# Kernel tuning notes

Hardware: AMD Instinct MI355X
Metric: run time of the kernel (lower is better)

Reference implementation:

```python
import jax, jax.numpy as jnp
import numpy as np
from jax import lax

BATCH, SEQ, D_FSQ = 8, 4096, 4
D_MODEL, D_STATE, D_CONV, L, OUT = 256, 16, 4, 2, 2
D_INNER = 2 * D_MODEL  # expand=2
EPS = 1e-5


def setup_inputs() -> dict:
    key = jax.random.key(0)
    ks = jax.random.split(key, 10)
    s = 0.02
    return {
        "z_seq": jax.random.normal(ks[0], (BATCH, SEQ, D_FSQ), jnp.float32),
        "ip_w": jax.random.normal(ks[1], (D_MODEL, D_FSQ), jnp.float32) * s,
        "ip_b": jnp.zeros((D_MODEL,), jnp.float32),
        "norm_g": jnp.ones((L, D_MODEL), jnp.float32),
        "norm_b": jnp.zeros((L, D_MODEL), jnp.float32),
        "inproj_w": jax.random.normal(ks[2], (L, 2 * D_INNER, D_MODEL), jnp.float32) * s,
        "conv_w": jax.random.normal(ks[3], (L, D_INNER, D_CONV), jnp.float32) * s,
        "conv_b": jnp.zeros((L, D_INNER), jnp.float32),
        "xproj_w": jax.random.normal(ks[4], (L, 2 * D_STATE + 1, D_INNER), jnp.float32) * s,
        "dt_w": jax.random.normal(ks[5], (L, D_INNER), jnp.float32) * s,
        "dt_b": jnp.zeros((L, D_INNER), jnp.float32),
        "outproj_w": jax.random.normal(ks[6], (L, D_MODEL, D_INNER), jnp.float32) * s,
        "onorm_g": jnp.ones((D_MODEL,), jnp.float32),
        "onorm_b": jnp.zeros((D_MODEL,), jnp.float32),
        "op_w": jax.random.normal(ks[7], (OUT, D_MODEL), jnp.float32) * s,
        "op_b": jnp.zeros((OUT,), jnp.float32),
    }


def _layernorm(x, g, b):
    mu = jnp.mean(x, axis=-1, keepdims=True)
    var = jnp.mean(jnp.square(x - mu), axis=-1, keepdims=True)
    return (x - mu) * lax.rsqrt(var + EPS) * g + b


def _selective_scan(x, dt, Bm, Cm):
    # x, dt: [B,T,d_inner]; Bm, Cm: [B,T,d_state]
    A = -jnp.arange(1, D_STATE + 1, dtype=x.dtype)  # [d_state]

    def step(h, inp):
        x_t, dt_t, B_t, C_t = inp  # [B,di],[B,di],[B,ds],[B,ds]
        A_bar = jnp.exp(dt_t[:, :, None] * A)            # [B,di,ds]
        h = A_bar * h + (dt_t * x_t)[:, :, None] * B_t[:, None, :]
        y_t = jnp.einsum("bds,bs->bd", h, C_t)
        return h, y_t

    xs = (jnp.swapaxes(x, 0, 1), jnp.swapaxes(dt, 0, 1),
          jnp.swapaxes(Bm, 0, 1), jnp.swapaxes(Cm, 0, 1))
    h0 = jnp.zeros((x.shape[0], D_INNER, D_STATE), x.dtype)
    _, ys = lax.scan(step, h0, xs)
    return jnp.swapaxes(ys, 0, 1)  # [B,T,d_inner]


def _block(x, g, b, Wi, cw, cb, Wx, dw, db, Wo):
    res = x
    x = _layernorm(x, g, b)
    xz = x @ Wi.T                               # [B,T,2*d_inner]
    xp, z = xz[..., :D_INNER], xz[..., D_INNER:]
    # causal depthwise conv1d (padding=d_conv-1 then truncate == left pad)
    xc = lax.conv_general_dilated(
        jnp.swapaxes(xp, 1, 2), cw[:, None, :], window_strides=(1,),
        padding=[(D_CONV - 1, 0)], dimension_numbers=("NCH", "OIH", "NCH"),
        feature_group_count=D_INNER) + cb[None, :, None]
    xc = jax.nn.silu(jnp.swapaxes(xc, 1, 2))    # [B,T,d_inner]
    ssm = xc @ Wx.T                             # [B,T,2*ds+1]
    Bm = ssm[..., :D_STATE]
    Cm = ssm[..., D_STATE:2 * D_STATE]
    dt_raw = ssm[..., 2 * D_STATE:]             # [B,T,1]
    dt = jax.nn.softplus(dt_raw * dw + db)      # Linear(1, d_inner)
    y = _selective_scan(xc, dt, Bm, Cm)
    y = y * jax.nn.silu(z)
    y = y @ Wo.T
    return y + res


def reference(z_seq, ip_w, ip_b, norm_g, norm_b, inproj_w, conv_w, conv_b,
              xproj_w, dt_w, dt_b, outproj_w, onorm_g, onorm_b, op_w, op_b):
    x = z_seq @ ip_w.T + ip_b
    for l in range(L):
        x = _block(x, norm_g[l], norm_b[l], inproj_w[l], conv_w[l], conv_b[l],
                   xproj_w[l], dt_w[l], dt_b[l], outproj_w[l])
    x = _layernorm(x, onorm_g, onorm_b)
    return x @ op_w.T + op_b
```

## Files before the change

kernel.cpp:

```cpp
#include <hip/hip_runtime.h>
#include <cstddef>
#include <cstdint>

#define DEV __device__ __forceinline__

namespace {
constexpr int BATCH = 8;
constexpr int SEQL  = 4096;
constexpr int DM    = 256;
constexpr int DS    = 16;
constexpr int DI    = 512;
constexpr int NTOK  = BATCH * SEQL;
constexpr int TC    = 64;
constexpr int NCH   = SEQL / TC;
constexpr float EPSF = 1e-5f;

constexpr size_t OFF_X   = 0;
constexpr size_t OFF_XPB = OFF_X   + (size_t)NTOK * DM * 4;
constexpr size_t OFF_ZBB = OFF_XPB + (size_t)NTOK * DI * 2;
constexpr size_t OFF_XCB = OFF_ZBB + (size_t)NTOK * DI * 2;
constexpr size_t OFF_XLN = OFF_XCB + (size_t)NTOK * DI * 2;
constexpr size_t OFF_B   = OFF_XLN + (size_t)NTOK * DM * 2;
constexpr size_t OFF_C   = OFF_B   + (size_t)NTOK * DS * 4;
constexpr size_t OFF_DTR = OFF_C   + (size_t)NTOK * DS * 4;
constexpr size_t OFF_HE  = OFF_DTR + (size_t)NTOK * 4;
constexpr size_t OFF_DTC = OFF_HE  + (size_t)BATCH * DI * NCH * DS * 4;
constexpr size_t OFF_WBI = OFF_DTC + (size_t)BATCH * DI * NCH * 4;
constexpr size_t OFF_WBO = OFF_WBI + (size_t)2 * 2 * DI * DM * 2;
constexpr size_t OFF_WBX = OFF_WBO + (size_t)2 * DM * DI * 2;
constexpr size_t OFF_CWT = OFF_WBX + (size_t)2 * 48 * DI * 2;
constexpr size_t WBI_EL  = 2 * 2 * DI * DM;
constexpr size_t WBO_EL  = 2 * DM * DI;
}

typedef __attribute__((ext_vector_type(8))) short short8;
typedef __attribute__((ext_vector_type(4))) float f32x4;

DEV float sigmoidf_(float v) { return 1.0f / (1.0f + __expf(-v)); }
DEV float siluf_(float v)    { return v * sigmoidf_(v); }
DEV float softplusf_(float v) {
    return fmaxf(v, 0.0f) + __logf(1.0f + __expf(-fabsf(v)));
}
DEV float b2f(unsigned short u) {
    union { unsigned int i; float f; } c; c.i = ((unsigned int)u) << 16; return c.f;
}
DEV float4 b4f(ushort4 u) {
    return make_float4(b2f(u.x), b2f(u.y), b2f(u.z), b2f(u.w));
}
DEV unsigned short f2b(float f) {
    union { float f; unsigned int i; } c; c.f = f;
    unsigned int lsb = (c.i >> 16) & 1u;
    c.i += 0x7fffu + lsb;
    return (unsigned short)(c.i >> 16);
}
DEV void pows16(float p, float* pb) {
    float p2 = p * p, p4 = p2 * p2, p8 = p4 * p4;
    pb[0] = p;        pb[1] = p2;       pb[2] = p2 * p;      pb[3] = p4;
    pb[4] = p4 * p;   pb[5] = p4 * p2;  pb[6] = p4 * p2 * p; pb[7] = p8;
    pb[8] = p8 * p;   pb[9] = p8 * p2;  pb[10] = p8 * p2 * p; pb[11] = p8 * p4;
    pb[12] = p8 * p4 * p; pb[13] = p8 * p4 * p2; pb[14] = p8 * p4 * p2 * p; pb[15] = p8 * p8;
}
DEV void gload_lds16(const unsigned short* g, unsigned short* l) {
    __builtin_amdgcn_global_load_lds(
        (__attribute__((address_space(1))) void*)(g),
        (__attribute__((address_space(3))) void*)(l), 16, 0, 0);
}

__global__ void k_cvt(const float* __restrict__ src, unsigned short* __restrict__ dst, int n) {
    int g = (blockIdx.x * 256 + threadIdx.x) * 4;
    if (g >= n) return;
    float4 v = *(const float4*)(src + g);
    ushort4 o;
    o.x = f2b(v.x); o.y = f2b(v.y); o.z = f2b(v.z); o.w = f2b(v.w);
    *(ushort4*)(dst + g) = o;
}

__global__ void k_cvtx(const float* __restrict__ src, unsigned short* __restrict__ dst) {
    int idx = blockIdx.x * 256 + threadIdx.x;
    int l = idx / (48 * 512), r = (idx >> 9) % 48, cc = idx & 511;
    dst[idx] = (r < 33) ? f2b(src[(size_t)(l * 33 + r) * 512 + cc]) : (unsigned short)0;
}

__global__ void k_cvtc(const float* __restrict__ src, float* __restrict__ dst) {
    int idx = blockIdx.x * 256 + threadIdx.x;
    int l = idx >> 11, k = (idx >> 9) & 3, d = idx & 511;
    dst[idx] = src[(size_t)(l * DI + d) * 4 + k];
}

__global__ void k_inproj(const float* __restrict__ z, const float* __restrict__ w,
                         const float* __restrict__ bias, float* __restrict__ x) {
    int g = blockIdx.x * 256 + threadIdx.x;
    int i = g >> 8, m = g & 255;
    float4 zv = *(const float4*)(z + (size_t)i * 4);
    float4 wv = *(const float4*)(w + (size_t)m * 4);
    float r = bias[m];
    r = fmaf(zv.x, wv.x, r);
    r = fmaf(zv.y, wv.y, r);
    r = fmaf(zv.z, wv.z, r);
    r = fmaf(zv.w, wv.w, r);
    x[g] = r;
}

__global__ void k_lnrow(const float* __restrict__ x, const float* __restrict__ gam,
                        const float* __restrict__ bet, unsigned short* __restrict__ xln) {
    int lane = threadIdx.x & 63, wid = threadIdx.x >> 6;
    int i = blockIdx.x * 4 + wid;
    float4 v = *(const float4*)(x + (size_t)i * DM + lane * 4);
    float s = v.x + v.y + v.z + v.w;
    float q = v.x * v.x + v.y * v.y + v.z * v.z + v.w * v.w;
    #pragma unroll
    for (int m = 32; m; m >>= 1) { s += __shfl_xor(s, m, 64); q += __shfl_xor(q, m, 64); }
    float mu = s * (1.0f / DM);
    float rs = rsqrtf(q * (1.0f / DM) - mu * mu + EPSF);
    float4 g4 = *(const float4*)(gam + lane * 4);
    float4 b4 = *(const float4*)(bet + lane * 4);
    ushort4 o;
    o.x = f2b((v.x - mu) * rs * g4.x + b4.x);
    o.y = f2b((v.y - mu) * rs * g4.y + b4.y);
    o.z = f2b((v.z - mu) * rs * g4.z + b4.z);
    o.w = f2b((v.w - mu) * rs * g4.w + b4.w);
    *(ushort4*)(xln + (size_t)i * DM + lane * 4) = o;
}

__global__ __launch_bounds__(256) void k_gemm1(
    const unsigned short* __restrict__ A, const unsigned short* __restrict__ W,
    unsigned short* __restrict__ xpb, unsigned short* __restrict__ zbb) {
    __shared__ unsigned short As[128 * 32];
    __shared__ unsigned short Bs[128 * 32];
    int tid = threadIdx.x, lane = tid & 63, wid = tid >> 6;
    int tileN = blockIdx.x & 7, tileM = blockIdx.x >> 3;
    int i0 = tileM * 128, n0 = tileN * 128;
    f32x4 acc[4][4];
    #pragma unroll
    for (int mi = 0; mi < 4; mi++)
        #pragma unroll
        for (int ni = 0; ni < 4; ni++) acc[mi][ni] = (f32x4){0.f, 0.f, 0.f, 0.f};

    int srow = (wid << 5) + (lane >> 2);
    int sblk = lane & 3;
    const unsigned short* ga = A + (size_t)(i0 + srow) * 256 + sblk * 8;
    const unsigned short* gb = W + (size_t)(n0 + srow) * 256 + sblk * 8;
    unsigned short* la = As + (wid << 5) * 32;
    unsigned short* lb = Bs + (wid << 5) * 32;
    int ar = lane & 15, ab = lane >> 4;
    const short8* pa = (const short8*)(As + ((wid >> 1) * 64 + ar) * 32 + ab * 8);
    const short8* pb = (const short8*)(Bs + ((wid & 1) * 64 + ar) * 32 + ab * 8);

    for (int k0 = 0; k0 < 256; k0 += 32) {
        gload_lds16(ga + k0,            la);
        gload_lds16(ga + k0 + 16 * 256, la + 16 * 32);
        gload_lds16(gb + k0,            lb);
        gload_lds16(gb + k0 + 16 * 256, lb + 16 * 32);
        __syncthreads();
        short8 a[4], b[4];
        #pragma unroll
        for (int mi = 0; mi < 4; mi++) a[mi] = pa[mi * 64];
        #pragma unroll
        for (int ni = 0; ni < 4; ni++) b[ni] = pb[ni * 64];
        #pragma unroll
        for (int mi = 0; mi < 4; mi++)
            #pragma unroll
            for (int ni = 0; ni < 4; ni++)
                acc[mi][ni] = __builtin_amdgcn_mfma_f32_16x16x32_bf16(a[mi], b[ni], acc[mi][ni], 0, 0, 0);
        __syncthreads();
    }
    int wr = wid >> 1, wc = wid & 1;
    int rbase = i0 + wr * 64 + (lane >> 4) * 4;
    int cbase = n0 + wc * 64 + (lane & 15);
    unsigned short* dst = (n0 < 512) ? xpb : zbb;
    int coff = (n0 < 512) ? cbase : cbase - 512;
    #pragma unroll
    for (int mi = 0; mi < 4; mi++)
        #pragma unroll
        for (int ni = 0; ni < 4; ni++)
            #pragma unroll
            for (int j = 0; j < 4; j++)
                dst[(size_t)(rbase + mi * 16 + j) * 512 + coff + ni * 16] = f2b(acc[mi][ni][j]);
}

__global__ void k_conv(const unsigned short* __restrict__ xpb, const float* __restrict__ cwT,
                       const float* __restrict__ cb, unsigned short* __restrict__ xcb) {
    int g = blockIdx.x * 256 + threadIdx.x;
    int tg = g >> 7, dq = g & 127;
    int d = dq * 4;
    int i0 = tg * 8;
    float4 w0 = *(const float4*)(cwT + 0 * DI + d);
    float4 w1 = *(const float4*)(cwT + 1 * DI + d);
    float4 w2 = *(const float4*)(cwT + 2 * DI + d);
    float4 w3 = *(const float4*)(cwT + 3 * DI + d);
    float4 bi = *(const float4*)(cb + d);
    float4 x0, x1, x2;
    if ((i0 & (SEQL - 1)) != 0) {
        x0 = b4f(*(const ushort4*)(xpb + (size_t)(i0 - 3) * DI + d));
        x1 = b4f(*(const ushort4*)(xpb + (size_t)(i0 - 2) * DI + d));
        x2 = b4f(*(const ushort4*)(xpb + (size_t)(i0 - 1) * DI + d));
    } else {
        x0 = x1 = x2 = make_float4(0.f, 0.f, 0.f, 0.f);
    }
    #pragma unroll
    for (int tt = 0; tt < 8; tt++) {
        float4 xc = b4f(*(const ushort4*)(xpb + (size_t)(i0 + tt) * DI + d));
        float4 a = bi;
        a.x = fmaf(w0.x, x0.x, a.x); a.y = fmaf(w0.y, x0.y, a.y);
        a.z = fmaf(w0.z, x0.z, a.z); a.w = fmaf(w0.w, x0.w, a.w);
        a.x = fmaf(w1.x, x1.x, a.x); a.y = fmaf(w1.y, x1.y, a.y);
        a.z = fmaf(w1.z, x1.z, a.z); a.w = fmaf(w1.w, x1.w, a.w);
        a.x = fmaf(w2.x, x2.x, a.x); a.y = fmaf(w2.y, x2.y, a.y);
        a.z = fmaf(w2.z, x2.z, a.z); a.w = fmaf(w2.w, x2.w, a.w);
        a.x = fmaf(w3.x, xc.x, a.x); a.y = fmaf(w3.y, xc.y, a.y);
        a.z = fmaf(w3.z, xc.z, a.z); a.w = fmaf(w3.w, xc.w, a.w);
        ushort4 o;
        o.x = f2b(siluf_(a.x)); o.y = f2b(siluf_(a.y));
        o.z = f2b(siluf_(a.z)); o.w = f2b(siluf_(a.w));
        *(ushort4*)(xcb + (size_t)(i0 + tt) * DI + d) = o;
        x0 = x1; x1 = x2; x2 = xc;
    }
}

__global__ __launch_bounds__(256) void k_xprojm(
    const unsigned short* __restrict__ A, const unsigned short* __restrict__ W,
    float* __restrict__ Bm, float* __restrict__ Cm, float* __restrict__ dtr) {
    __shared__ unsigned short As[128 * 32];
    __shared__ unsigned short Bs[48 * 32];
    int tid = threadIdx.x, lane = tid & 63, wid = tid >> 6;
    int i0 = blockIdx.x * 128;
    f32x4 acc[2][3];
    #pragma unroll
    for (int mi = 0; mi < 2; mi++)
        #pragma unroll
        for (int ni = 0; ni < 3; ni++) acc[mi][ni] = (f32x4){0.f, 0.f, 0.f, 0.f};

    int srow = lane >> 2, sblk = lane & 3;
    const unsigned short* ga = A + (size_t)(i0 + (wid << 5) + srow) * 512 + sblk * 8;
    unsigned short* la = As + (wid << 5) * 32;
    const unsigned short* gb = W + (size_t)((wid << 4) + srow) * 512 + sblk * 8;
    unsigned short* lb = Bs + (wid << 4) * 32;
    int ar = lane & 15, ab = lane >> 4;

    for (int k0 = 0; k0 < 512; k0 += 32) {
        gload_lds16(ga + k0,            la);
        gload_lds16(ga + k0 + 16 * 512, la + 16 * 32);
        if (wid < 3) gload_lds16(gb + k0, lb);
        __syncthreads();
        short8 a[2], b[3];
        #pragma unroll
        for (int mi = 0; mi < 2; mi++)
            a[mi] = *(const short8*)(As + ((wid << 5) + mi * 16 + ar) * 32 + ab * 8);
        #pragma unroll
        for (int ni = 0; ni < 3; ni++)
            b[ni] = *(const short8*)(Bs + (ni * 16 + ar) * 32 + ab * 8);
        #pragma unroll
        for (int mi = 0; mi < 2; mi++)
            #pragma unroll
            for (int ni = 0; ni < 3; ni++)
                acc[mi][ni] = __builtin_amdgcn_mfma_f32_16x16x32_bf16(a[mi], b[ni], acc[mi][ni], 0, 0, 0);
        __syncthreads();
    }
    #pragma unroll
    for (int mi = 0; mi < 2; mi++)
        #pragma unroll
        for (int ni = 0; ni < 3; ni++)
            #pragma unroll
            for (int j = 0; j < 4; j++) {
                int row = i0 + (wid << 5) + mi * 16 + (lane >> 4) * 4 + j;
                int ng = ni * 16 + (lane & 15);
                float v = acc[mi][ni][j];
                if (ng < 16)       Bm[(size_t)row * DS + ng] = v;
                else if (ng < 32)  Cm[(size_t)row * DS + ng - 16] = v;
                else if (ng == 32) dtr[row] = v;
            }
}

__global__ __launch_bounds__(256) void k_scan1(
    const unsigned short* __restrict__ xcb, const float* __restrict__ Bm,
    const float* __restrict__ dtr, const float* __restrict__ dw,
    const float* __restrict__ db, float* __restrict__ hend, float* __restrict__ dtc) {
    __shared__ float Bsh[64][16];
    __shared__ float dtl[64];
    int tid = threadIdx.x;
    int blk = blockIdx.x;
    int half = blk & 1, c = (blk >> 1) & (NCH - 1), b = blk >> 7;
    int d = half * 256 + tid;
    int i0 = (b << 12) + c * TC;
    if (tid < 64) dtl[tid] = dtr[i0 + tid];
    {
        int idx = tid * 4, tt = idx >> 4, ss = idx & 15;
        *(float4*)(&Bsh[tt][ss]) = *(const float4*)(Bm + (size_t)(i0 + tt) * DS + ss);
    }
    __syncthreads();
    float dwd = dw[d], dbd = db[d];
    float h[16];
    #pragma unroll
    for (int s = 0; s < 16; s++) h[s] = 0.0f;
    float dtsum = 0.0f;
    for (int t = 0; t < TC; t++) {
        float dt = softplusf_(fmaf(dtl[t], dwd, dbd));
        dtsum += dt;
        float p = __expf(-dt);
        float pb[16];
        pows16(p, pb);
        float x = b2f(xcb[(size_t)(i0 + t) * DI + d]);
        float dtx = dt * x;
        float Bv[16];
        *(float4*)(Bv + 0)  = *(const float4*)(&Bsh[t][0]);
        *(float4*)(Bv + 4)  = *(const float4*)(&Bsh[t][4]);
        *(float4*)(Bv + 8)  = *(const float4*)(&Bsh[t][8]);
        *(float4*)(Bv + 12) = *(const float4*)(&Bsh[t][12]);
        #pragma unroll
        for (int s = 0; s < 16; s++) h[s] = fmaf(pb[s], h[s], dtx * Bv[s]);
    }
    size_t hb = ((size_t)(b * DI + d) * NCH + c) * DS;
    #pragma unroll
    for (int s = 0; s < 16; s += 4)
        *(float4*)(hend + hb + s) = make_float4(h[s], h[s + 1], h[s + 2], h[s + 3]);
    dtc[(size_t)(b * DI + d) * NCH + c] = dtsum;
}

__global__ void k_scan2(float* __restrict__ hend, const float* __restrict__ dtc) {
    int g = blockIdx.x * 256 + threadIdx.x;
    int s = g & 15, dd = (g >> 4) & 511, b = g >> 13;
    size_t base = (size_t)(b * DI + dd) * NCH;
    float hin = 0.0f;
    float kneg = -(float)(s + 1);
    #pragma unroll 4
    for (int c = 0; c < NCH; c++) {
        size_t a = (base + c) * DS + s;
        float tmp = hend[a];
        float pb = __expf(kneg * dtc[base + c]);
        hend[a] = hin;
        hin = fmaf(pb, hin, tmp);
    }
}

__global__ __launch_bounds__(256) void k_scan3(
    const unsigned short* __restrict__ xcb, const float* __restrict__ Bm,
    const float* __restrict__ Cm, const float* __restrict__ dtr,
    const float* __restrict__ dw, const float* __restrict__ db,
    const float* __restrict__ hend, const unsigned short* __restrict__ zbb,
    unsigned short* __restrict__ ygb) {
    __shared__ float Bsh[64][16];
    __shared__ float Csh[64][16];
    __shared__ float dtl[64];
    int tid = threadIdx.x;
    int blk = blockIdx.x;
    int half = blk & 1, c = (blk >> 1) & (NCH - 1), b = blk >> 7;
    int d = half * 256 + tid;
    int i0 = (b << 12) + c * TC;
    if (tid < 64) dtl[tid] = dtr[i0 + tid];
    {
        int idx = tid * 4, tt = idx >> 4, ss = idx & 15;
        *(float4*)(&Bsh[tt][ss]) = *(const float4*)(Bm + (size_t)(i0 + tt) * DS + ss);
        *(float4*)(&Csh[tt][ss]) = *(const float4*)(Cm + (size_t)(i0 + tt) * DS + ss);
    }
    __syncthreads();
    float dwd = dw[d], dbd = db[d];
    float h[16];
    size_t hb = ((size_t)(b * DI + d) * NCH + c) * DS;
    #pragma unroll
    for (int s = 0; s < 16; s += 4) *(float4*)(h + s) = *(const float4*)(hend + hb + s);
    for (int t = 0; t < TC; t++) {
        float dt = softplusf_(fmaf(dtl[t], dwd, dbd));
        float p = __expf(-dt);
        float pb[16];
        pows16(p, pb);
        size_t gi = (size_t)(i0 + t) * DI + d;
        float x = b2f(xcb[gi]);
        float dtx = dt * x;
        float Bv[16], Cv[16];
        *(float4*)(Bv + 0)  = *(const float4*)(&Bsh[t][0]);
        *(float4*)(Bv + 4)  = *(const float4*)(&Bsh[t][4]);
        *(float4*)(Bv + 8)  = *(const float4*)(&Bsh[t][8]);
        *(float4*)(Bv + 12) = *(const float4*)(&Bsh[t][12]);
        *(float4*)(Cv + 0)  = *(const float4*)(&Csh[t][0]);
        *(float4*)(Cv + 4)  = *(const float4*)(&Csh[t][4]);
        *(float4*)(Cv + 8)  = *(const float4*)(&Csh[t][8]);
        *(float4*)(Cv + 12) = *(const float4*)(&Csh[t][12]);
        float y = 0.0f;
        #pragma unroll
        for (int s = 0; s < 16; s++) {
            h[s] = fmaf(pb[s], h[s], dtx * Bv[s]);
            y = fmaf(h[s], Cv[s], y);
        }
        float z = b2f(zbb[gi]);
        ygb[gi] = f2b(y * siluf_(z));
    }
}

__global__ __launch_bounds__(256) void k_outproj(
    const unsigned short* __restrict__ A, const unsigned short* __restrict__ W,
    float* __restrict__ x) {
    __shared__ unsigned short As[128 * 32];
    __shared__ unsigned short Bs[128 * 32];
    int tid = threadIdx.x, lane = tid & 63, wid = tid >> 6;
    int tileN = blockIdx.x & 1, tileM = blockIdx.x >> 1;
    int i0 = tileM * 128, n0 = tileN * 128;
    f32x4 acc[4][4];
    #pragma unroll
    for (int mi = 0; mi < 4; mi++)
        #pragma unroll
        for (int ni = 0; ni < 4; ni++) acc[mi][ni] = (f32x4){0.f, 0.f, 0.f, 0.f};

    int srow = (wid << 5) + (lane >> 2);
    int sblk = lane & 3;
    const unsigned short* ga = A + (size_t)(i0 + srow) * 512 + sblk * 8;
    const unsigned short* gb = W + (size_t)(n0 + srow) * 512 + sblk * 8;
    unsigned short* la = As + (wid << 5) * 32;
    unsigned short* lb = Bs + (wid << 5) * 32;
    int ar = lane & 15, ab = lane >> 4;
    const short8* pa = (const short8*)(As + ((wid >> 1) * 64 + ar) * 32 + ab * 8);
    const short8* pb = (const short8*)(Bs + ((wid & 1) * 64 + ar) * 32 + ab * 8);

    for (int k0 = 0; k0 < 512; k0 += 32) {
        gload_lds16(ga + k0,            la);
        gload_lds16(ga + k0 + 16 * 512, la + 16 * 32);
        gload_lds16(gb + k0,            lb);
        gload_lds16(gb + k0 + 16 * 512, lb + 16 * 32);
        __syncthreads();
        short8 a[4], b[4];
        #pragma unroll
        for (int mi = 0; mi < 4; mi++) a[mi] = pa[mi * 64];
        #pragma unroll
        for (int ni = 0; ni < 4; ni++) b[ni] = pb[ni * 64];
        #pragma unroll
        for (int mi = 0; mi < 4; mi++)
            #pragma unroll
            for (int ni = 0; ni < 4; ni++)
                acc[mi][ni] = __builtin_amdgcn_mfma_f32_16x16x32_bf16(a[mi], b[ni], acc[mi][ni], 0, 0, 0);
        __syncthreads();
    }
    int wr = wid >> 1, wc = wid & 1;
    int rbase = i0 + wr * 64 + (lane >> 4) * 4;
    int cbase = n0 + wc * 64 + (lane & 15);
    #pragma unroll
    for (int mi = 0; mi < 4; mi++)
        #pragma unroll
        for (int ni = 0; ni < 4; ni++)
            #pragma unroll
            for (int j = 0; j < 4; j++) {
                size_t idx = (size_t)(rbase + mi * 16 + j) * DM + cbase + ni * 16;
                x[idx] += acc[mi][ni][j];
            }
}

__global__ void k_final(const float* __restrict__ x, const float* __restrict__ gam,
                        const float* __restrict__ bet, const float* __restrict__ w,
                        const float* __restrict__ bias, float* __restrict__ out) {
    int lane = threadIdx.x & 63, wid = threadIdx.x >> 6;
    int i = blockIdx.x * 4 + wid;
    float4 v = *(const float4*)(x + (size_t)i * DM + lane * 4);
    float s = v.x + v.y + v.z + v.w;
    float q = v.x * v.x + v.y * v.y + v.z * v.z + v.w * v.w;
    #pragma unroll
    for (int m = 32; m; m >>= 1) { s += __shfl_xor(s, m, 64); q += __shfl_xor(q, m, 64); }
    float mu = s * (1.0f / DM);
    float rs = rsqrtf(q * (1.0f / DM) - mu * mu + EPSF);
    float4 gg = *(const float4*)(gam + lane * 4);
    float4 bb = *(const float4*)(bet + lane * 4);
    float xn[4] = {(v.x - mu) * rs * gg.x + bb.x, (v.y - mu) * rs * gg.y + bb.y,
                   (v.z - mu) * rs * gg.z + bb.z, (v.w - mu) * rs * gg.w + bb.w};
    float4 w0 = *(const float4*)(w + lane * 4);
    float4 w1 = *(const float4*)(w + DM + lane * 4);
    float p0 = xn[0] * w0.x + xn[1] * w0.y + xn[2] * w0.z + xn[3] * w0.w;
    float p1 = xn[0] * w1.x + xn[1] * w1.y + xn[2] * w1.z + xn[3] * w1.w;
    #pragma unroll
    for (int m = 32; m; m >>= 1) { p0 += __shfl_xor(p0, m, 64); p1 += __shfl_xor(p1, m, 64); }
    if (lane == 0) {
        out[(size_t)i * 2]     = p0 + bias[0];
        out[(size_t)i * 2 + 1] = p1 + bias[1];
    }
}

extern "C" void kernel_launch(void* const* d_in, const int* in_sizes, int n_in,
                              void* d_out, int out_size, void* d_ws, size_t ws_size,
                              hipStream_t stream) {
    const float* z_seq     = (const float*)d_in[0];
    const float* ip_w      = (const float*)d_in[1];
    const float* ip_b      = (const float*)d_in[2];
    const float* norm_g    = (const float*)d_in[3];
    const float* norm_b    = (const float*)d_in[4];
    const float* inproj_w  = (const float*)d_in[5];
    const float* conv_w    = (const float*)d_in[6];
    const float* conv_b    = (const float*)d_in[7];
    const float* xproj_w   = (const float*)d_in[8];
    const float* dt_w      = (const float*)d_in[9];
    const float* dt_b      = (const float*)d_in[10];
    const float* outproj_w = (const float*)d_in[11];
    const float* onorm_g   = (const float*)d_in[12];
    const float* onorm_b   = (const float*)d_in[13];
    const float* op_w      = (const float*)d_in[14];
    const float* op_b      = (const float*)d_in[15];

    char* ws = (char*)d_ws;
    float* x    = (float*)(ws + OFF_X);
    unsigned short* xpb = (unsigned short*)(ws + OFF_XPB);
    unsigned short* zbb = (unsigned short*)(ws + OFF_ZBB);
    unsigned short* xcb = (unsigned short*)(ws + OFF_XCB);
    unsigned short* xln = (unsigned short*)(ws + OFF_XLN);
    float* Bmb  = (float*)(ws + OFF_B);
    float* Cmb  = (float*)(ws + OFF_C);
    float* dtrb = (float*)(ws + OFF_DTR);
    float* hend = (float*)(ws + OFF_HE);
    float* dtc  = (float*)(ws + OFF_DTC);
    unsigned short* WbI = (unsigned short*)(ws + OFF_WBI);
    unsigned short* WbO = (unsigned short*)(ws + OFF_WBO);
    unsigned short* WbX = (unsigned short*)(ws + OFF_WBX);
    float* cwT  = (float*)(ws + OFF_CWT);

    k_cvt<<<(int)(WBI_EL / 4 / 256), 256, 0, stream>>>(inproj_w,  WbI, (int)WBI_EL);
    k_cvt<<<(int)(WBO_EL / 4 / 256), 256, 0, stream>>>(outproj_w, WbO, (int)WBO_EL);
    k_cvtx<<<2 * 48 * 512 / 256, 256, 0, stream>>>(xproj_w, WbX);
    k_cvtc<<<2 * 4 * 512 / 256, 256, 0, stream>>>(conv_w, cwT);

    k_inproj<<<NTOK * DM / 256, 256, 0, stream>>>(z_seq, ip_w, ip_b, x);

    for (int l = 0; l < 2; l++) {
        k_lnrow<<<NTOK / 4, 256, 0, stream>>>(x, norm_g + l * DM, norm_b + l * DM, xln);
        k_gemm1<<<(NTOK / 128) * 8, 256, 0, stream>>>(
            xln, WbI + (size_t)l * 2 * DI * DM, xpb, zbb);
        k_conv<<<(NTOK / 8) * 128 / 256, 256, 0, stream>>>(
            xpb, cwT + (size_t)l * 4 * DI, conv_b + (size_t)l * DI, xcb);
        k_xprojm<<<NTOK / 128, 256, 0, stream>>>(
            xcb, WbX + (size_t)l * 48 * DI, Bmb, Cmb, dtrb);
        k_scan1<<<BATCH * NCH * 2, 256, 0, stream>>>(
            xcb, Bmb, dtrb, dt_w + l * DI, dt_b + l * DI, hend, dtc);
        k_scan2<<<BATCH * DI * DS / 256, 256, 0, stream>>>(hend, dtc);
        k_scan3<<<BATCH * NCH * 2, 256, 0, stream>>>(
            xcb, Bmb, Cmb, dtrb, dt_w + l * DI, dt_b + l * DI, hend, zbb, xpb);
        k_outproj<<<(NTOK / 128) * 2, 256, 0, stream>>>(
            xpb, WbO + (size_t)l * DM * DI, x);
    }
    k_final<<<NTOK / 4, 256, 0, stream>>>(x, onorm_g, onorm_b, op_w, op_b, (float*)d_out);
}
```

Before: 509.0 us.

## Halve scan chunk length, process two channels per thread, fuse softplus with decay

The scan chunk length drops from 64 to 32, which doubles the number of chunks. Each scan thread now handles two adjacent channels, using vectorized ushort2 loads and stores for x, z and y, and one launch covers all 512 channels per chunk. Softplus and the exp(-dt) decay are now computed together as p = rcp(1+e^a) and dt = -log(p), which saves a transcendental per step. In exchange, register pressure goes up, and the serial inter-chunk pass in k_scan2 runs twice as long. The fused formula can also lose precision or overflow for large dt arguments.

```diff
diff --git a/kernel.cpp b/kernel.cpp
--- a/kernel.cpp
+++ b/kernel.cpp
@@ -11,7 +11,7 @@
 constexpr int DS    = 16;
 constexpr int DI    = 512;
 constexpr int NTOK  = BATCH * SEQL;
-constexpr int TC    = 64;
+constexpr int TC    = 32;
 constexpr int NCH   = SEQL / TC;
 constexpr float EPSF = 1e-5f;
 
@@ -38,9 +38,6 @@
 
 DEV float sigmoidf_(float v) { return 1.0f / (1.0f + __expf(-v)); }
 DEV float siluf_(float v)    { return v * sigmoidf_(v); }
-DEV float softplusf_(float v) {
-    return fmaxf(v, 0.0f) + __logf(1.0f + __expf(-fabsf(v)));
-}
 DEV float b2f(unsigned short u) {
     union { unsigned int i; float f; } c; c.i = ((unsigned int)u) << 16; return c.f;
 }
@@ -52,6 +49,10 @@
     unsigned int lsb = (c.i >> 16) & 1u;
     c.i += 0x7fffu + lsb;
     return (unsigned short)(c.i >> 16);
+}
+DEV void dt_p_(float a, float& dt, float& p) {
+    p = __builtin_amdgcn_rcpf(1.0f + __expf(a));
+    dt = -__logf(p);
 }
 DEV void pows16(float p, float* pb) {
     float p2 = p * p, p4 = p2 * p2, p8 = p4 * p4;
@@ -271,49 +272,58 @@
             }
 }
 
-__global__ __launch_bounds__(256) void k_scan1(
+__global__ __launch_bounds__(256, 4) void k_scan1(
     const unsigned short* __restrict__ xcb, const float* __restrict__ Bm,
     const float* __restrict__ dtr, const float* __restrict__ dw,
     const float* __restrict__ db, float* __restrict__ hend, float* __restrict__ dtc) {
-    __shared__ float Bsh[64][16];
-    __shared__ float dtl[64];
+    __shared__ float Bsh[TC][16];
+    __shared__ float dtl[TC];
     int tid = threadIdx.x;
     int blk = blockIdx.x;
-    int half = blk & 1, c = (blk >> 1) & (NCH - 1), b = blk >> 7;
-    int d = half * 256 + tid;
+    int c = blk & (NCH - 1), b = blk >> 7;
+    int d0 = tid * 2;
     int i0 = (b << 12) + c * TC;
-    if (tid < 64) dtl[tid] = dtr[i0 + tid];
-    {
-        int idx = tid * 4, tt = idx >> 4, ss = idx & 15;
+    if (tid < TC) dtl[tid] = dtr[i0 + tid];
+    if (tid < TC * 4) {
+        int tt = tid >> 2, ss = (tid & 3) * 4;
         *(float4*)(&Bsh[tt][ss]) = *(const float4*)(Bm + (size_t)(i0 + tt) * DS + ss);
     }
     __syncthreads();
-    float dwd = dw[d], dbd = db[d];
-    float h[16];
-    #pragma unroll
-    for (int s = 0; s < 16; s++) h[s] = 0.0f;
-    float dtsum = 0.0f;
+    float2 dwd = *(const float2*)(dw + d0);
+    float2 dbd = *(const float2*)(db + d0);
+    float h0[16], h1[16];
+    #pragma unroll
+    for (int s = 0; s < 16; s++) { h0[s] = 0.0f; h1[s] = 0.0f; }
+    float dts0 = 0.0f, dts1 = 0.0f;
     for (int t = 0; t < TC; t++) {
-        float dt = softplusf_(fmaf(dtl[t], dwd, dbd));
-        dtsum += dt;
-        float p = __expf(-dt);
-        float pb[16];
-        pows16(p, pb);
-        float x = b2f(xcb[(size_t)(i0 + t) * DI + d]);
-        float dtx = dt * x;
+        float dt0, p0, dt1, p1;
+        dt_p_(fmaf(dtl[t], dwd.x, dbd.x), dt0, p0);
+        dt_p_(fmaf(dtl[t], dwd.y, dbd.y), dt1, p1);
+        dts0 += dt0; dts1 += dt1;
+        ushort2 xv = *(const ushort2*)(xcb + (size_t)(i0 + t) * DI + d0);
+        float dtx0 = dt0 * b2f(xv.x);
+        float dtx1 = dt1 * b2f(xv.y);
         float Bv[16];
         *(float4*)(Bv + 0)  = *(const float4*)(&Bsh[t][0]);
         *(float4*)(Bv + 4)  = *(const float4*)(&Bsh[t][4]);
         *(float4*)(Bv + 8)  = *(const float4*)(&Bsh[t][8]);
         *(float4*)(Bv + 12) = *(const float4*)(&Bsh[t][12]);
-        #pragma unroll
-        for (int s = 0; s < 16; s++) h[s] = fmaf(pb[s], h[s], dtx * Bv[s]);
-    }
-    size_t hb = ((size_t)(b * DI + d) * NCH + c) * DS;
-    #pragma unroll
-    for (int s = 0; s < 16; s += 4)
-        *(float4*)(hend + hb + s) = make_float4(h[s], h[s + 1], h[s + 2], h[s + 3]);
-    dtc[(size_t)(b * DI + d) * NCH + c] = dtsum;
+        float pb[16];
+        pows16(p0, pb);
+        #pragma unroll
+        for (int s = 0; s < 16; s++) h0[s] = fmaf(pb[s], h0[s], dtx0 * Bv[s]);
+        pows16(p1, pb);
+        #pragma unroll
+        for (int s = 0; s < 16; s++) h1[s] = fmaf(pb[s], h1[s], dtx1 * Bv[s]);
+    }
+    size_t hb0 = ((size_t)(b * DI + d0) * NCH + c) * DS;
+    #pragma unroll
+    for (int s = 0; s < 16; s += 4) {
+        *(float4*)(hend + hb0 + s)      = make_float4(h0[s], h0[s+1], h0[s+2], h0[s+3]);
+        *(float4*)(hend + hb0 + DS * NCH + s) = make_float4(h1[s], h1[s+1], h1[s+2], h1[s+3]);
+    }
+    dtc[(size_t)(b * DI + d0) * NCH + c] = dts0;
+    dtc[(size_t)(b * DI + d0 + 1) * NCH + c] = dts1;
 }
 
 __global__ void k_scan2(float* __restrict__ hend, const float* __restrict__ dtc) {
@@ -332,40 +342,47 @@
     }
 }
 
-__global__ __launch_bounds__(256) void k_scan3(
+__global__ __launch_bounds__(256, 4) void k_scan3(
     const unsigned short* __restrict__ xcb, const float* __restrict__ Bm,
     const float* __restrict__ Cm, const float* __restrict__ dtr,
     const float* __restrict__ dw, const float* __restrict__ db,
     const float* __restrict__ hend, const unsigned short* __restrict__ zbb,
     unsigned short* __restrict__ ygb) {
-    __shared__ float Bsh[64][16];
-    __shared__ float Csh[64][16];
-    __shared__ float dtl[64];
+    __shared__ float Bsh[TC][16];
+    __shared__ float Csh[TC][16];
+    __shared__ float dtl[TC];
     int tid = threadIdx.x;
     int blk = blockIdx.x;
-    int half = blk & 1, c = (blk >> 1) & (NCH - 1), b = blk >> 7;
-    int d = half * 256 + tid;
+    int c = blk & (NCH - 1), b = blk >> 7;
+    int d0 = tid * 2;
     int i0 = (b << 12) + c * TC;
-    if (tid < 64) dtl[tid] = dtr[i0 + tid];
-    {
-        int idx = tid * 4, tt = idx >> 4, ss = idx & 15;
+    if (tid < TC) dtl[tid] = dtr[i0 + tid];
+    if (tid < TC * 4) {
+        int tt = tid >> 2, ss = (tid & 3) * 4;
         *(float4*)(&Bsh[tt][ss]) = *(const float4*)(Bm + (size_t)(i0 + tt) * DS + ss);
+    } else if (tid < TC * 8) {
+        int q = tid - TC * 4;
+        int tt = q >> 2, ss = (q & 3) * 4;
         *(float4*)(&Csh[tt][ss]) = *(const float4*)(Cm + (size_t)(i0 + tt) * DS + ss);
     }
     __syncthreads();
-    float dwd = dw[d], dbd = db[d];
-    float h[16];
-    size_t hb = ((size_t)(b * DI + d) * NCH + c) * DS;
-    #pragma unroll
-    for (int s = 0; s < 16; s += 4) *(float4*)(h + s) = *(const float4*)(hend + hb + s);
+    float2 dwd = *(const float2*)(dw + d0);
+    float2 dbd = *(const float2*)(db + d0);
+    float h0[16], h1[16];
+    size_t hb0 = ((size_t)(b * DI + d0) * NCH + c) * DS;
+    #pragma unroll
+    for (int s = 0; s < 16; s += 4) {
+        *(float4*)(h0 + s) = *(const float4*)(hend + hb0 + s);
+        *(float4*)(h1 + s) = *(const float4*)(hend + hb0 + DS * NCH + s);
+    }
     for (int t = 0; t < TC; t++) {
-        float dt = softplusf_(fmaf(dtl[t], dwd, dbd));
-        float p = __expf(-dt);
-        float pb[16];
-        pows16(p, pb);
-        size_t gi = (size_t)(i0 + t) * DI + d;
-        float x = b2f(xcb[gi]);
-        float dtx = dt * x;
+        float dt0, p0, dt1, p1;
+        dt_p_(fmaf(dtl[t], dwd.x, dbd.x), dt0, p0);
+        dt_p_(fmaf(dtl[t], dwd.y, dbd.y), dt1, p1);
+        size_t gi = (size_t)(i0 + t) * DI + d0;
+        ushort2 xv = *(const ushort2*)(xcb + gi);
+        float dtx0 = dt0 * b2f(xv.x);
+        float dtx1 = dt1 * b2f(xv.y);
         float Bv[16], Cv[16];
         *(float4*)(Bv + 0)  = *(const float4*)(&Bsh[t][0]);
         *(float4*)(Bv + 4)  = *(const float4*)(&Bsh[t][4]);
@@ -375,14 +392,25 @@
         *(float4*)(Cv + 4)  = *(const float4*)(&Csh[t][4]);
         *(float4*)(Cv + 8)  = *(const float4*)(&Csh[t][8]);
         *(float4*)(Cv + 12) = *(const float4*)(&Csh[t][12]);
-        float y = 0.0f;
+        float pb[16];
+        float y0 = 0.0f, y1 = 0.0f;
+        pows16(p0, pb);
         #pragma unroll
         for (int s = 0; s < 16; s++) {
-            h[s] = fmaf(pb[s], h[s], dtx * Bv[s]);
-            y = fmaf(h[s], Cv[s], y);
+            h0[s] = fmaf(pb[s], h0[s], dtx0 * Bv[s]);
+            y0 = fmaf(h0[s], Cv[s], y0);
         }
-        float z = b2f(zbb[gi]);
-        ygb[gi] = f2b(y * siluf_(z));
+        pows16(p1, pb);
+        #pragma unroll
+        for (int s = 0; s < 16; s++) {
+            h1[s] = fmaf(pb[s], h1[s], dtx1 * Bv[s]);
+            y1 = fmaf(h1[s], Cv[s], y1);
+        }
+        ushort2 zv = *(const ushort2*)(zbb + gi);
+        ushort2 o;
+        o.x = f2b(y0 * siluf_(b2f(zv.x)));
+        o.y = f2b(y1 * siluf_(b2f(zv.y)));
+        *(ushort2*)(ygb + gi) = o;
     }
 }
 
@@ -521,10 +549,10 @@
             xpb, cwT + (size_t)l * 4 * DI, conv_b + (size_t)l * DI, xcb);
         k_xprojm<<<NTOK / 128, 256, 0, stream>>>(
             xcb, WbX + (size_t)l * 48 * DI, Bmb, Cmb, dtrb);
-        k_scan1<<<BATCH * NCH * 2, 256, 0, stream>>>(
+        k_scan1<<<BATCH * NCH, 256, 0, stream>>>(
             xcb, Bmb, dtrb, dt_w + l * DI, dt_b + l * DI, hend, dtc);
         k_scan2<<<BATCH * DI * DS / 256, 256, 0, stream>>>(hend, dtc);
-        k_scan3<<<BATCH * NCH * 2, 256, 0, stream>>>(
+        k_scan3<<<BATCH * NCH, 256, 0, stream>>>(
             xcb, Bmb, Cmb, dtrb, dt_w + l * DI, dt_b + l * DI, hend, zbb, xpb);
         k_outproj<<<(NTOK / 128) * 2, 256, 0, stream>>>(
             xpb, WbO + (size_t)l * DM * DI, x);
```

After: 547.2 us. +7.5%, slower.
